# Performance work log

Hardware: AMD Instinct MI355X
Metric: run time of the kernel (lower is better)

## Reference

```python
import jax, jax.numpy as jnp
import numpy as np

N_NODES = 50000
N_EDGES = 800000
NODE_C = 128
EDGE_C = 64


def setup_inputs() -> dict:
    key = jax.random.key(0)
    ks = jax.random.split(key, 12)
    x_nodes = jax.random.normal(ks[0], (N_NODES, NODE_C), dtype=jnp.float32)
    x_edges = jax.random.normal(ks[1], (N_EDGES, EDGE_C), dtype=jnp.float32)
    edge_index = jax.random.randint(ks[2], (2, N_EDGES), 0, N_NODES, dtype=jnp.int64)
    def lin(k, fan_in, fan_out):
        # torch Linear default init: U(-1/sqrt(fan_in), 1/sqrt(fan_in))
        b = 1.0 / np.sqrt(fan_in)
        kw, kb = jax.random.split(k)
        W = jax.random.uniform(kw, (fan_in, fan_out), minval=-b, maxval=b, dtype=jnp.float32)
        bias = jax.random.uniform(kb, (fan_out,), minval=-b, maxval=b, dtype=jnp.float32)
        return W, bias
    eW1, eb1 = lin(ks[3], 2 * NODE_C + EDGE_C, NODE_C)
    eW2, eb2 = lin(ks[4], NODE_C, EDGE_C)
    nW1, nb1 = lin(ks[5], NODE_C + EDGE_C, NODE_C)
    nW2, nb2 = lin(ks[6], NODE_C, NODE_C)
    return {
        "x_nodes": x_nodes, "x_edges": x_edges, "edge_index": edge_index,
        "eW1": eW1, "eb1": eb1, "eW2": eW2, "eb2": eb2,
        "nW1": nW1, "nb1": nb1, "nW2": nW2, "nb2": nb2,
    }


def reference(x_nodes, x_edges, edge_index, eW1, eb1, eW2, eb2, nW1, nb1, nW2, nb2):
    sender, receiver = edge_index[0], edge_index[1]
    # gather + concat: [E, 2*node_c + edge_c]
    state = jnp.concatenate((x_nodes[sender], x_nodes[receiver], x_edges), axis=1)
    # edge MLP: Linear -> SiLU -> Linear -> SiLU
    h = jax.nn.silu(state @ eW1 + eb1)
    x_edges_out = jax.nn.silu(h @ eW2 + eb2)
    # scatter_add into receiver nodes
    aggr = jax.ops.segment_sum(x_edges_out, receiver, num_segments=x_nodes.shape[0])
    # node MLP: Linear -> SiLU -> Linear
    n = jnp.concatenate((x_nodes, aggr), axis=1)
    x_nodes_out = jax.nn.silu(n @ nW1 + nb1) @ nW2 + nb2
    return (x_nodes_out, x_edges_out)
```

## Files before the change

kernel.cpp:

```cpp
#include <hip/hip_runtime.h>
#include <hip/hip_bf16.h>

#define E_N    800000
#define NODES  50000
#define NC     128
#define EC     64
#define H1     128
#define O2E    64
#define NK1    192

typedef __fp16 half2_t __attribute__((ext_vector_type(2)));

__device__ __forceinline__ unsigned short f2h_rne(float f) {
    union { _Float16 h; unsigned short s; } v; v.h = (_Float16)f; return v.s;
}
__device__ __forceinline__ float h2f(unsigned short s) {
    union { unsigned short s; _Float16 h; } v; v.s = s; return (float)v.h;
}
__device__ __forceinline__ unsigned int packh2(float a, float b) {
    return (unsigned int)f2h_rne(a) | ((unsigned int)f2h_rne(b) << 16);
}
__device__ __forceinline__ unsigned int pkrtz(float a, float b) {
    union { half2_t h; unsigned int u; } v;
    v.h = __builtin_amdgcn_cvt_pkrtz(a, b);
    return v.u;
}
__device__ __forceinline__ half2_t u2h2(unsigned int u) {
    union { unsigned int u; half2_t h; } v; v.u = u; return v.h;
}
#define FDOT2(a, b, c) __builtin_amdgcn_fdot2(u2h2(a), u2h2(b), (c), false)

__device__ __forceinline__ float silu_f(float x) { return x / (1.0f + __expf(-x)); }

__global__ __launch_bounds__(256, 2) void pre_kernel(
    const float* __restrict__ xn,
    const float* __restrict__ eW1,
    const float* __restrict__ eb1,
    unsigned short* __restrict__ pa,
    unsigned short* __restrict__ pb)
{
    const int t    = threadIdx.x;
    const int col  = t & 127;
    const int half = t >> 7;
    const int row0 = half * NC;

    float w[128];
    #pragma unroll
    for (int k = 0; k < 128; ++k)
        w[k] = eW1[(size_t)(row0 + k) * H1 + col];
    const float bias = half ? 0.0f : eb1[col];

    __shared__ __align__(16) float4 sx[NC / 4];

    unsigned short* __restrict__ dst = half ? pb : pa;

    float4 x4a = make_float4(0.f, 0.f, 0.f, 0.f);
    if (t < 32) x4a = ((const float4*)(xn + (size_t)blockIdx.x * NC))[t];

    for (int v = blockIdx.x; v < NODES; v += gridDim.x) {
        const int vn    = v + gridDim.x;
        const int vload = (vn < NODES) ? vn : v;
        if (t < 32) {
            sx[t] = x4a;
            x4a = ((const float4*)(xn + (size_t)vload * NC))[t];
        }
        __syncthreads();

        float a0 = 0.f, a1 = 0.f, a2 = 0.f, a3 = 0.f;
        #pragma unroll
        for (int j = 0; j < 32; ++j) {
            float4 x = sx[j];
            a0 = fmaf(w[4 * j + 0], x.x, a0);
            a1 = fmaf(w[4 * j + 1], x.y, a1);
            a2 = fmaf(w[4 * j + 2], x.z, a2);
            a3 = fmaf(w[4 * j + 3], x.w, a3);
        }
        float r = (a0 + a1) + (a2 + a3) + bias;
        dst[(size_t)v * NC + col] = f2h_rne(r);
        __syncthreads();
    }
}

__global__ __launch_bounds__(256, 4) void edge_kernel(
    const float* __restrict__ xe,
    const int* __restrict__ ei,
    const unsigned short* __restrict__ pa,
    const unsigned short* __restrict__ pb,
    const float* __restrict__ eW1,
    const float* __restrict__ eW2,
    const float* __restrict__ eb2,
    float* __restrict__ out_e,
    float* __restrict__ aggr)
{
    const int t   = threadIdx.x;
    const int sub = t >> 7;
    const int c   = t & 127;
    const int o   = t & 63;
    const int q   = (t >> 6) & 1;

    unsigned int w1p[32];
    #pragma unroll
    for (int j = 0; j < 32; ++j)
        w1p[j] = packh2(eW1[(size_t)(256 + 2 * j) * H1 + c],
                        eW1[(size_t)(256 + 2 * j + 1) * H1 + c]);
    unsigned int w2p[32];
    #pragma unroll
    for (int j = 0; j < 32; ++j)
        w2p[j] = packh2(eW2[(size_t)(q * 64 + 2 * j) * O2E + o],
                        eW2[(size_t)(q * 64 + 2 * j + 1) * O2E + o]);
    const float b2v = eb2[o];

    __shared__ __align__(16) uint2        xbufp[2][16];
    __shared__ __align__(16) unsigned int hbufp[2][64];
    __shared__ float                      red[2][O2E];

    const int stride = gridDim.x * 2;

    int rcv_c;
    unsigned short pav_c, pbv_c;
    float4 x4 = make_float4(0.f, 0.f, 0.f, 0.f);
    {
        const int e0  = blockIdx.x * 2 + sub;
        const int snd = ei[e0];
        rcv_c = ei[E_N + e0];
        pav_c = pa[(size_t)snd * NC + c];
        pbv_c = pb[(size_t)rcv_c * NC + c];
        if (c < 16) x4 = ((const float4*)(xe + (size_t)e0 * EC))[c];
    }

    for (int base = blockIdx.x * 2; base < E_N; base += stride) {
        const int e_cur   = base + sub;
        const int rcv_cur = rcv_c;
        const unsigned short pav = pav_c, pbv = pbv_c;

        const int basen = base + stride;
        const int en    = (basen < E_N) ? (basen + sub) : e_cur;

        if (c < 16)
            xbufp[sub][c] = make_uint2(pkrtz(x4.x, x4.y), pkrtz(x4.z, x4.w));
        const int snd_n = ei[en];
        const int rcv_n = ei[E_N + en];
        if (c < 16) x4 = ((const float4*)(xe + (size_t)en * EC))[c];

        __syncthreads();

        float a0 = 0.f, a1 = 0.f;
        {
            const uint4* xp = (const uint4*)xbufp[sub];
            #pragma unroll
            for (int j = 0; j < 8; ++j) {
                uint4 u = xp[j];
                a0 = FDOT2(u.x, w1p[4 * j + 0], a0);
                a1 = FDOT2(u.y, w1p[4 * j + 1], a1);
                a0 = FDOT2(u.z, w1p[4 * j + 2], a0);
                a1 = FDOT2(u.w, w1p[4 * j + 3], a1);
            }
        }
        float h = silu_f(a0 + a1 + h2f(pav) + h2f(pbv));

        float hx = __shfl_xor(h, 1);
        unsigned int hpk = (c & 1) ? pkrtz(hx, h) : pkrtz(h, hx);
        if (!(c & 1)) hbufp[sub][c >> 1] = hpk;

        pav_c = pa[(size_t)snd_n * NC + c];
        pbv_c = pb[(size_t)rcv_n * NC + c];
        rcv_c = rcv_n;

        __syncthreads();

        float d0 = 0.f, d1 = 0.f;
        {
            const uint4* hp4 = ((const uint4*)hbufp[sub]) + q * 8;
            #pragma unroll
            for (int j = 0; j < 8; ++j) {
                uint4 u = hp4[j];
                d0 = FDOT2(u.x, w2p[4 * j + 0], d0);
                d1 = FDOT2(u.y, w2p[4 * j + 1], d1);
                d0 = FDOT2(u.z, w2p[4 * j + 2], d0);
                d1 = FDOT2(u.w, w2p[4 * j + 3], d1);
            }
        }
        float acc2 = d0 + d1;
        if (q) red[sub][o] = acc2;
        __syncthreads();
        if (!q) {
            float ov = silu_f(acc2 + red[sub][o] + b2v);
            out_e[(size_t)e_cur * O2E + o] = ov;
            unsafeAtomicAdd(&aggr[(size_t)rcv_cur * O2E + o], ov);
        }
    }
}

__global__ __launch_bounds__(256, 3) void node_kernel(
    const float* __restrict__ xn,
    const float* __restrict__ aggr,
    const float* __restrict__ nW1, const float* __restrict__ nb1,
    const float* __restrict__ nW2, const float* __restrict__ nb2,
    float* __restrict__ out_n)
{
    const int t  = threadIdx.x;
    const int c  = t & 127;
    const int kh = t >> 7;

    unsigned int w1p[48];
    {
        const int k0 = kh * 96;
        #pragma unroll
        for (int j = 0; j < 48; ++j)
            w1p[j] = packh2(nW1[(size_t)(k0 + 2 * j) * NC + c],
                            nW1[(size_t)(k0 + 2 * j + 1) * NC + c]);
    }
    unsigned int w2p[32];
    {
        const int k0 = kh * 64;
        #pragma unroll
        for (int j = 0; j < 32; ++j)
            w2p[j] = packh2(nW2[(size_t)(k0 + 2 * j) * NC + c],
                            nW2[(size_t)(k0 + 2 * j + 1) * NC + c]);
    }
    const float b1 = nb1[c];
    const float b2 = nb2[c];

    __shared__ __align__(16) uint2        sbufp[48];
    __shared__ float                      red1[NC];
    __shared__ __align__(16) unsigned int hbufp[64];

    float4 x4a = make_float4(0.f, 0.f, 0.f, 0.f);
    if (t < 32)       x4a = ((const float4*)(xn + (size_t)blockIdx.x * NC))[t];
    else if (t < 48)  x4a = ((const float4*)(aggr + (size_t)blockIdx.x * EC))[t - 32];

    for (int v = blockIdx.x; v < NODES; v += gridDim.x) {
        const int vn    = v + gridDim.x;
        const int vload = (vn < NODES) ? vn : v;

        if (t < 48) {
            sbufp[t] = make_uint2(pkrtz(x4a.x, x4a.y), pkrtz(x4a.z, x4a.w));
            x4a = (t < 32)
                ? ((const float4*)(xn + (size_t)vload * NC))[t]
                : ((const float4*)(aggr + (size_t)vload * EC))[t - 32];
        }
        __syncthreads();

        float a0 = 0.f, a1 = 0.f;
        {
            const uint4* sp = ((const uint4*)sbufp) + kh * 12;
            #pragma unroll
            for (int j = 0; j < 12; ++j) {
                uint4 u = sp[j];
                a0 = FDOT2(u.x, w1p[4 * j + 0], a0);
                a1 = FDOT2(u.y, w1p[4 * j + 1], a1);
                a0 = FDOT2(u.z, w1p[4 * j + 2], a0);
                a1 = FDOT2(u.w, w1p[4 * j + 3], a1);
            }
        }
        float acc = a0 + a1;
        if (kh) red1[c] = acc;
        __syncthreads();

        if (!kh) {
            float h  = silu_f(acc + red1[c] + b1);
            float hx = __shfl_xor(h, 1);
            unsigned int hpk = (c & 1) ? pkrtz(hx, h) : pkrtz(h, hx);
            if (!(c & 1)) hbufp[c >> 1] = hpk;
        }
        __syncthreads();

        float d0 = 0.f, d1 = 0.f;
        {
            const uint4* hp4 = ((const uint4*)hbufp) + kh * 8;
            #pragma unroll
            for (int j = 0; j < 8; ++j) {
                uint4 u = hp4[j];
                d0 = FDOT2(u.x, w2p[4 * j + 0], d0);
                d1 = FDOT2(u.y, w2p[4 * j + 1], d1);
                d0 = FDOT2(u.z, w2p[4 * j + 2], d0);
                d1 = FDOT2(u.w, w2p[4 * j + 3], d1);
            }
        }
        float acc2 = d0 + d1;
        if (kh) red1[c] = acc2;
        __syncthreads();
        if (!kh) out_n[(size_t)v * NC + c] = acc2 + red1[c] + b2;
    }
}

extern "C" void kernel_launch(void* const* d_in, const int* in_sizes, int n_in,
                              void* d_out, int out_size, void* d_ws, size_t ws_size,
                              hipStream_t stream) {
    const float* xn  = (const float*)d_in[0];
    const float* xe  = (const float*)d_in[1];
    const int*   ei  = (const int*)d_in[2];
    const float* eW1 = (const float*)d_in[3];
    const float* eb1 = (const float*)d_in[4];
    const float* eW2 = (const float*)d_in[5];
    const float* eb2 = (const float*)d_in[6];
    const float* nW1 = (const float*)d_in[7];
    const float* nb1 = (const float*)d_in[8];
    const float* nW2 = (const float*)d_in[9];
    const float* nb2 = (const float*)d_in[10];

    float* out_n = (float*)d_out;
    float* out_e = out_n + (size_t)NODES * NC;
    float* aggr  = (float*)d_ws;

    unsigned short* pa = (unsigned short*)out_n;
    unsigned short* pb = pa + (size_t)NODES * NC;

    (void)hipMemsetAsync(aggr, 0, (size_t)NODES * O2E * sizeof(float), stream);

    hipLaunchKernelGGL(pre_kernel, dim3(1024), dim3(256), 0, stream,
                       xn, eW1, eb1, pa, pb);
    hipLaunchKernelGGL(edge_kernel, dim3(1024), dim3(256), 0, stream,
                       xe, ei, pa, pb, eW1, eW2, eb2, out_e, aggr);
    hipLaunchKernelGGL(node_kernel, dim3(1024), dim3(256), 0, stream,
                       xn, aggr, nW1, nb1, nW2, nb2, out_n);
}
```

Baseline: 1.011 ms.

## Tile edge MLP into 32-edge blocks using MFMA f16 matrix instructions

Rewrites the edge kernel so each block processes 32 edges per iteration, with both edge-MLP matmuls done by 16x16x16 f16 MFMA instructions instead of per-thread fdot2 loops over 2 edges. The precomputed sender and receiver projections are gathered with vector loads, pre-summed in half precision, and staged in padded LDS tiles. The aim is to cut ALU work and per-edge barrier overhead. It costs more LDS and registers, and the half-precision add of the projections loses some precision. It also adds a trailing barrier in the node kernel's loop.

Result: slower. 1.216 ms (+20.2%).

```diff
diff --git a/kernel.cpp b/kernel.cpp
--- a/kernel.cpp
+++ b/kernel.cpp
@@ -1,5 +1,4 @@
 #include <hip/hip_runtime.h>
-#include <hip/hip_bf16.h>
 
 #define E_N    800000
 #define NODES  50000
@@ -8,8 +7,11 @@
 #define H1     128
 #define O2E    64
 #define NK1    192
+#define NTILES (E_N / 32)
 
 typedef __fp16 half2_t __attribute__((ext_vector_type(2)));
+typedef __fp16 half4_t __attribute__((ext_vector_type(4)));
+typedef float  f32x4   __attribute__((ext_vector_type(4)));
 
 __device__ __forceinline__ unsigned short f2h_rne(float f) {
     union { _Float16 h; unsigned short s; } v; v.h = (_Float16)f; return v.s;
@@ -28,7 +30,12 @@
 __device__ __forceinline__ half2_t u2h2(unsigned int u) {
     union { unsigned int u; half2_t h; } v; v.u = u; return v.h;
 }
+__device__ __forceinline__ unsigned int hadd2(unsigned int a, unsigned int b) {
+    union { unsigned int u; half2_t h; } x, y;
+    x.u = a; y.u = b; x.h = x.h + y.h; return x.u;
+}
 #define FDOT2(a, b, c) __builtin_amdgcn_fdot2(u2h2(a), u2h2(b), (c), false)
+#define MFMA16(a, b, c) __builtin_amdgcn_mfma_f32_16x16x16f16((a), (b), (c), 0, 0, 0)
 
 __device__ __forceinline__ float silu_f(float x) { return x / (1.0f + __expf(-x)); }
 
@@ -93,101 +100,153 @@
     float* __restrict__ aggr)
 {
     const int t   = threadIdx.x;
-    const int sub = t >> 7;
-    const int c   = t & 127;
-    const int o   = t & 63;
-    const int q   = (t >> 6) & 1;
-
-    unsigned int w1p[32];
+    const int l   = t & 63;
+    const int w   = t >> 6;
+    const int l16 = l & 15;
+    const int g   = l >> 4;
+    const int es  = t >> 3;
+    const int d   = t & 7;
+
+    half4_t a1[2][4];
     #pragma unroll
-    for (int j = 0; j < 32; ++j)
-        w1p[j] = packh2(eW1[(size_t)(256 + 2 * j) * H1 + c],
-                        eW1[(size_t)(256 + 2 * j + 1) * H1 + c]);
-    unsigned int w2p[32];
+    for (int m = 0; m < 2; ++m) {
+        const int ch = (2 * w + m) * 16 + l16;
+        #pragma unroll
+        for (int ks = 0; ks < 4; ++ks) {
+            #pragma unroll
+            for (int i = 0; i < 4; ++i)
+                a1[m][ks][i] = (__fp16)eW1[(size_t)(256 + ks * 16 + 4 * g + i) * H1 + ch];
+        }
+    }
+    half4_t a2[8];
+    {
+        const int o = w * 16 + l16;
+        #pragma unroll
+        for (int ks = 0; ks < 8; ++ks)
+            #pragma unroll
+            for (int i = 0; i < 4; ++i)
+                a2[ks][i] = (__fp16)eW2[(size_t)(ks * 16 + 4 * g + i) * O2E + o];
+    }
+    const int o0 = w * 16 + 4 * g;
+    float b2b[4];
     #pragma unroll
-    for (int j = 0; j < 32; ++j)
-        w2p[j] = packh2(eW2[(size_t)(q * 64 + 2 * j) * O2E + o],
-                        eW2[(size_t)(q * 64 + 2 * j + 1) * O2E + o]);
-    const float b2v = eb2[o];
-
-    __shared__ __align__(16) uint2        xbufp[2][16];
-    __shared__ __align__(16) unsigned int hbufp[2][64];
-    __shared__ float                      red[2][O2E];
-
-    const int stride = gridDim.x * 2;
-
-    int rcv_c;
-    unsigned short pav_c, pbv_c;
-    float4 x4 = make_float4(0.f, 0.f, 0.f, 0.f);
+    for (int r = 0; r < 4; ++r) b2b[r] = eb2[o0 + r];
+
+    __shared__ __align__(16) unsigned int xe_lds[32 * 36];
+    __shared__ __align__(16) unsigned int ps_lds[32 * 68];
+    __shared__ __align__(16) unsigned int h_lds [32 * 68];
+    __shared__ int rcv_lds[32];
+
+    uint4 pa0, pa1, pb0, pb1;
+    float4 xf0, xf1;
+    int rcv_r = 0;
+
     {
-        const int e0  = blockIdx.x * 2 + sub;
-        const int snd = ei[e0];
-        rcv_c = ei[E_N + e0];
-        pav_c = pa[(size_t)snd * NC + c];
-        pbv_c = pb[(size_t)rcv_c * NC + c];
-        if (c < 16) x4 = ((const float4*)(xe + (size_t)e0 * EC))[c];
-    }
-
-    for (int base = blockIdx.x * 2; base < E_N; base += stride) {
-        const int e_cur   = base + sub;
-        const int rcv_cur = rcv_c;
-        const unsigned short pav = pav_c, pbv = pbv_c;
-
-        const int basen = base + stride;
-        const int en    = (basen < E_N) ? (basen + sub) : e_cur;
-
-        if (c < 16)
-            xbufp[sub][c] = make_uint2(pkrtz(x4.x, x4.y), pkrtz(x4.z, x4.w));
-        const int snd_n = ei[en];
-        const int rcv_n = ei[E_N + en];
-        if (c < 16) x4 = ((const float4*)(xe + (size_t)en * EC))[c];
-
-        __syncthreads();
-
-        float a0 = 0.f, a1 = 0.f;
+        const int en  = blockIdx.x * 32 + es;
+        const int snd = ei[en];
+        rcv_r = ei[E_N + en];
+        const uint4* par = (const uint4*)(pa + (size_t)snd * NC);
+        pa0 = par[d * 2]; pa1 = par[d * 2 + 1];
+        const uint4* pbr = (const uint4*)(pb + (size_t)rcv_r * NC);
+        pb0 = pbr[d * 2]; pb1 = pbr[d * 2 + 1];
+        const float4* xr = (const float4*)(xe + (size_t)en * EC);
+        xf0 = xr[d * 2]; xf1 = xr[d * 2 + 1];
+    }
+
+    for (int tl = blockIdx.x; tl < NTILES; tl += gridDim.x) {
         {
-            const uint4* xp = (const uint4*)xbufp[sub];
-            #pragma unroll
-            for (int j = 0; j < 8; ++j) {
-                uint4 u = xp[j];
-                a0 = FDOT2(u.x, w1p[4 * j + 0], a0);
-                a1 = FDOT2(u.y, w1p[4 * j + 1], a1);
-                a0 = FDOT2(u.z, w1p[4 * j + 2], a0);
-                a1 = FDOT2(u.w, w1p[4 * j + 3], a1);
-            }
-        }
-        float h = silu_f(a0 + a1 + h2f(pav) + h2f(pbv));
-
-        float hx = __shfl_xor(h, 1);
-        unsigned int hpk = (c & 1) ? pkrtz(hx, h) : pkrtz(h, hx);
-        if (!(c & 1)) hbufp[sub][c >> 1] = hpk;
-
-        pav_c = pa[(size_t)snd_n * NC + c];
-        pbv_c = pb[(size_t)rcv_n * NC + c];
-        rcv_c = rcv_n;
-
-        __syncthreads();
-
-        float d0 = 0.f, d1 = 0.f;
-        {
-            const uint4* hp4 = ((const uint4*)hbufp[sub]) + q * 8;
-            #pragma unroll
-            for (int j = 0; j < 8; ++j) {
-                uint4 u = hp4[j];
-                d0 = FDOT2(u.x, w2p[4 * j + 0], d0);
-                d1 = FDOT2(u.y, w2p[4 * j + 1], d1);
-                d0 = FDOT2(u.z, w2p[4 * j + 2], d0);
-                d1 = FDOT2(u.w, w2p[4 * j + 3], d1);
-            }
-        }
-        float acc2 = d0 + d1;
-        if (q) red[sub][o] = acc2;
-        __syncthreads();
-        if (!q) {
-            float ov = silu_f(acc2 + red[sub][o] + b2v);
-            out_e[(size_t)e_cur * O2E + o] = ov;
-            unsafeAtomicAdd(&aggr[(size_t)rcv_cur * O2E + o], ov);
-        }
+            uint4 xp;
+            xp.x = pkrtz(xf0.x, xf0.y); xp.y = pkrtz(xf0.z, xf0.w);
+            xp.z = pkrtz(xf1.x, xf1.y); xp.w = pkrtz(xf1.z, xf1.w);
+            *(uint4*)&xe_lds[es * 36 + d * 4] = xp;
+            uint4 s0, s1;
+            s0.x = hadd2(pa0.x, pb0.x); s0.y = hadd2(pa0.y, pb0.y);
+            s0.z = hadd2(pa0.z, pb0.z); s0.w = hadd2(pa0.w, pb0.w);
+            s1.x = hadd2(pa1.x, pb1.x); s1.y = hadd2(pa1.y, pb1.y);
+            s1.z = hadd2(pa1.z, pb1.z); s1.w = hadd2(pa1.w, pb1.w);
+            *(uint4*)&ps_lds[es * 68 + d * 8]     = s0;
+            *(uint4*)&ps_lds[es * 68 + d * 8 + 4] = s1;
+            if (d == 0) rcv_lds[es] = rcv_r;
+        }
+        __syncthreads();
+
+        const int tn = tl + (int)gridDim.x;
+        if (tn < NTILES) {
+            const int en  = tn * 32 + es;
+            const int snd = ei[en];
+            rcv_r = ei[E_N + en];
+            const uint4* par = (const uint4*)(pa + (size_t)snd * NC);
+            pa0 = par[d * 2]; pa1 = par[d * 2 + 1];
+            const uint4* pbr = (const uint4*)(pb + (size_t)rcv_r * NC);
+            pb0 = pbr[d * 2]; pb1 = pbr[d * 2 + 1];
+            const float4* xr = (const float4*)(xe + (size_t)en * EC);
+            xf0 = xr[d * 2]; xf1 = xr[d * 2 + 1];
+        }
+
+        f32x4 acc[2][2];
+        #pragma unroll
+        for (int m = 0; m < 2; ++m)
+            #pragma unroll
+            for (int n = 0; n < 2; ++n)
+                acc[m][n] = (f32x4){0.f, 0.f, 0.f, 0.f};
+        #pragma unroll
+        for (int n = 0; n < 2; ++n) {
+            const unsigned int* xrow = &xe_lds[(n * 16 + l16) * 36];
+            #pragma unroll
+            for (int ks = 0; ks < 4; ++ks) {
+                half4_t b = *(const half4_t*)&xrow[ks * 8 + 2 * g];
+                acc[0][n] = MFMA16(a1[0][ks], b, acc[0][n]);
+                acc[1][n] = MFMA16(a1[1][ks], b, acc[1][n]);
+            }
+        }
+        #pragma unroll
+        for (int m = 0; m < 2; ++m) {
+            const int chu = (2 * w + m) * 8 + 2 * g;
+            #pragma unroll
+            for (int n = 0; n < 2; ++n) {
+                const int erow = n * 16 + l16;
+                union { uint2 u; unsigned short s[4]; } pu;
+                pu.u = *(const uint2*)&ps_lds[erow * 68 + chu];
+                float h0 = silu_f(acc[m][n][0] + h2f(pu.s[0]));
+                float h1 = silu_f(acc[m][n][1] + h2f(pu.s[1]));
+                float h2 = silu_f(acc[m][n][2] + h2f(pu.s[2]));
+                float h3 = silu_f(acc[m][n][3] + h2f(pu.s[3]));
+                uint2 hp; hp.x = pkrtz(h0, h1); hp.y = pkrtz(h2, h3);
+                *(uint2*)&h_lds[erow * 68 + chu] = hp;
+            }
+        }
+        __syncthreads();
+
+        f32x4 acc2[2];
+        acc2[0] = (f32x4){0.f, 0.f, 0.f, 0.f};
+        acc2[1] = (f32x4){0.f, 0.f, 0.f, 0.f};
+        #pragma unroll
+        for (int n = 0; n < 2; ++n) {
+            const unsigned int* hrow = &h_lds[(n * 16 + l16) * 68];
+            #pragma unroll
+            for (int ks = 0; ks < 8; ++ks) {
+                half4_t b = *(const half4_t*)&hrow[ks * 8 + 2 * g];
+                acc2[n] = MFMA16(a2[ks], b, acc2[n]);
+            }
+        }
+        #pragma unroll
+        for (int n = 0; n < 2; ++n) {
+            const int erow = n * 16 + l16;
+            const int eg   = tl * 32 + erow;
+            const int rcv  = rcv_lds[erow];
+            float4 ov;
+            ov.x = silu_f(acc2[n][0] + b2b[0]);
+            ov.y = silu_f(acc2[n][1] + b2b[1]);
+            ov.z = silu_f(acc2[n][2] + b2b[2]);
+            ov.w = silu_f(acc2[n][3] + b2b[3]);
+            *(float4*)&out_e[(size_t)eg * O2E + o0] = ov;
+            float* ag = &aggr[(size_t)rcv * O2E + o0];
+            unsafeAtomicAdd(ag + 0, ov.x);
+            unsafeAtomicAdd(ag + 1, ov.y);
+            unsafeAtomicAdd(ag + 2, ov.z);
+            unsafeAtomicAdd(ag + 3, ov.w);
+        }
+        __syncthreads();
     }
 }
 
@@ -281,6 +340,7 @@
         if (kh) red1[c] = acc2;
         __syncthreads();
         if (!kh) out_n[(size_t)v * NC + c] = acc2 + red1[c] + b2;
+        __syncthreads();
     }
 }
 
```
